# Kernel optimization log

Measured on AMD Instinct MI355X. Metric: run time of the kernel, lower is better.

Reference implementation:

```python
import jax, jax.numpy as jnp
import numpy as np

HEADS = 5 - 1  # 4 attention heads (GPSConv heads=4)


def _bn(x, g, b, eps=1e-5):
    # BatchNorm1d, training-mode math (biased variance), matches torch normalization
    mu = x.mean(0)
    var = x.var(0)
    return g * (x - mu) * jax.lax.rsqrt(var + eps) + b


def _forward(x, t, freqs, t_fc1_W, t_fc1_b, t_fc2_W, t_fc2_b, node_W, node_b,
             tproj_W, tproj_b, tcat_W, tcat_b, pen_g, pen_b, pel_W, pel_b,
             cat_W, cat_b, conv_Wg, gru_Wih, gru_bih, gru_Whh, gru_bhh,
             attn_Wqkv, attn_bqkv, attn_Wo, attn_bo, bn_g, bn_b,
             mlp_W1, mlp_b1, mlp_W2, mlp_b2, out_W, out_b):
    B, C, Hh, Ww = x.shape
    HD = node_W.shape[1]          # hidden_dim = 64
    DH = HD // HEADS              # per-head dim = 16
    WL = pen_g.shape[0]           # walk_length = 20

    xf = x.reshape(B, -1)                              # [B, D]
    h = xf @ node_W + node_b                           # node_proj

    # TimeEmbedding: t @ freqs -> sin/cos -> MLP, then time_proj
    tp = t.reshape(B, 1) * freqs.reshape(1, -1)        # [B, nf]
    two_pi = jnp.asarray(2.0 * np.pi, x.dtype)
    te = jnp.concatenate([jnp.sin(two_pi * tp), jnp.cos(two_pi * tp)], axis=-1)
    te = jax.nn.silu(te @ t_fc1_W + t_fc1_b) @ t_fc2_W + t_fc2_b
    h_time = te @ tproj_W + tproj_b
    h = jnp.concatenate([h, h_time], axis=-1) @ tcat_W + tcat_b  # time_cat_proj

    # Fully-connected graph incl. self-loops: A = 1 everywhere, deg = B.
    # Random-walk PE: P = A/deg has all entries 1/B; P is idempotent (P@P = P),
    # hence diag(P^k) = diag(P) = 1/B for every k in 1..walk_length.
    A = jnp.ones((B, B), x.dtype)
    P = A / A.sum(1, keepdims=True)
    pe = jnp.broadcast_to(jnp.diagonal(P)[:, None], (B, WL))
    pe = _bn(pe, pen_g, pen_b)                         # pe_norm (batch stats)
    h = jnp.concatenate([h, pe @ pel_W + pel_b], axis=-1) @ cat_W + cat_b

    inv_sqrt = jnp.asarray(1.0 / np.sqrt(DH), x.dtype)
    for l in range(conv_Wg.shape[0]):                  # 5 GPSConv layers
        # --- GatedGraphConv (num_layers=1): message, add-aggregate, GRU ---
        m = A @ (h @ conv_Wg[l])                       # sum of messages from all src nodes
        gi = m @ gru_Wih[l] + gru_bih[l]               # [B, 3H]
        gh = h @ gru_Whh[l] + gru_bhh[l]
        ir, iz, inn = jnp.split(gi, 3, axis=-1)
        hr, hz, hn = jnp.split(gh, 3, axis=-1)
        r = jax.nn.sigmoid(ir + hr)
        z = jax.nn.sigmoid(iz + hz)
        n = jnp.tanh(inn + r * hn)
        hc = (1.0 - z) * n + z * h                     # GRUCell output
        h1 = _bn(hc + h, bn_g[l, 0], bn_b[l, 0])       # residual + norm1

        # --- global multihead self-attention over the single dense batch ---
        qkv = h @ attn_Wqkv[l] + attn_bqkv[l]
        q, k, v = jnp.split(qkv, 3, axis=-1)
        q = q.reshape(B, HEADS, DH).transpose(1, 0, 2)  # [h, B, d]
        k = k.reshape(B, HEADS, DH).transpose(1, 0, 2)
        v = v.reshape(B, HEADS, DH).transpose(1, 0, 2)
        att = jax.nn.softmax(jnp.einsum('hqd,hkd->hqk', q, k) * inv_sqrt, axis=-1)
        o = jnp.einsum('hqk,hkd->hqd', att, v).transpose(1, 0, 2).reshape(B, HD)
        o = o @ attn_Wo[l] + attn_bo[l]
        h2 = _bn(o + h, bn_g[l, 1], bn_b[l, 1])        # residual + norm2

        s = h1 + h2
        s = s + (jax.nn.relu(s @ mlp_W1[l] + mlp_b1[l]) @ mlp_W2[l] + mlp_b2[l])
        h = _bn(s, bn_g[l, 2], bn_b[l, 2])             # norm3

    return (h @ out_W + out_b).reshape(B, C, Hh, Ww)


def setup_inputs() -> dict:
    key = jax.random.key(0)
    B, C, H, W = 2048, 4, 32, 32
    D = C * H * W                 # 4096
    HD, PE, WL, L = 64, 16, 20, 5
    NF, TH, TC = 8, 64, 64
    ks = iter(jax.random.split(key, 40))

    def rn(shape, s=0.05):
        return jax.random.normal(next(ks), shape, jnp.float32) * s

    return {
        'x': jax.random.normal(next(ks), (B, C, H, W), jnp.float32),
        't': jax.random.uniform(next(ks), (B,), jnp.float32),
        'freqs': rn((NF,), 1.0),
        't_fc1_W': rn((2 * NF, TH)), 't_fc1_b': rn((TH,)),
        't_fc2_W': rn((TH, TC)), 't_fc2_b': rn((TC,)),
        'node_W': rn((D, HD), 0.02), 'node_b': rn((HD,)),
        'tproj_W': rn((TC, HD)), 'tproj_b': rn((HD,)),
        'tcat_W': rn((2 * HD, HD)), 'tcat_b': rn((HD,)),
        'pen_g': jnp.ones((WL,), jnp.float32), 'pen_b': jnp.zeros((WL,), jnp.float32),
        'pel_W': rn((WL, PE)), 'pel_b': rn((PE,)),
        'cat_W': rn((HD + PE, HD)), 'cat_b': rn((HD,)),
        'conv_Wg': rn((L, HD, HD)),
        'gru_Wih': rn((L, HD, 3 * HD)), 'gru_bih': rn((L, 3 * HD)),
        'gru_Whh': rn((L, HD, 3 * HD)), 'gru_bhh': rn((L, 3 * HD)),
        'attn_Wqkv': rn((L, HD, 3 * HD)), 'attn_bqkv': rn((L, 3 * HD)),
        'attn_Wo': rn((L, HD, HD)), 'attn_bo': rn((L, HD)),
        'bn_g': jnp.ones((L, 3, HD), jnp.float32), 'bn_b': jnp.zeros((L, 3, HD), jnp.float32),
        'mlp_W1': rn((L, HD, 2 * HD)), 'mlp_b1': rn((L, 2 * HD)),
        'mlp_W2': rn((L, 2 * HD, HD)), 'mlp_b2': rn((L, HD)),
        'out_W': rn((HD, D)), 'out_b': rn((D,)),
    }


def reference(x, t, freqs, t_fc1_W, t_fc1_b, t_fc2_W, t_fc2_b, node_W, node_b,
              tproj_W, tproj_b, tcat_W, tcat_b, pen_g, pen_b, pel_W, pel_b,
              cat_W, cat_b, conv_Wg, gru_Wih, gru_bih, gru_Whh, gru_bhh,
              attn_Wqkv, attn_bqkv, attn_Wo, attn_bo, bn_g, bn_b,
              mlp_W1, mlp_b1, mlp_W2, mlp_b2, out_W, out_b):
    return _forward(x, t, freqs, t_fc1_W, t_fc1_b, t_fc2_W, t_fc2_b, node_W, node_b,
                    tproj_W, tproj_b, tcat_W, tcat_b, pen_g, pen_b, pel_W, pel_b,
                    cat_W, cat_b, conv_Wg, gru_Wih, gru_bih, gru_Whh, gru_bhh,
                    attn_Wqkv, attn_bqkv, attn_Wo, attn_bo, bn_g, bn_b,
                    mlp_W1, mlp_b1, mlp_W2, mlp_b2, out_W, out_b)
```

## Files before the change

### kernel.cpp

```cpp
#include <hip/hip_runtime.h>

#define NB 2048
#define HDM 64
#define NLAY 5

typedef __bf16 bf16x8 __attribute__((ext_vector_type(8)));
typedef float v4f __attribute__((ext_vector_type(4)));

__device__ __forceinline__ float sigmoidf_(float x){ return 1.f/(1.f+__expf(-x)); }
__device__ __forceinline__ float tanhfast_(float x){
  x = fminf(fmaxf(x, -15.f), 15.f);
  float e = __expf(2.f*x);
  return (e-1.f)/(e+1.f);
}
__device__ __forceinline__ unsigned short f2b_rne(float f){
  unsigned u = __float_as_uint(f);
  unsigned r = u + 0x7FFFu + ((u>>16)&1u);
  return (unsigned short)(r>>16);
}
__device__ __forceinline__ unsigned pk2(float a, float b){
  unsigned ua = (__float_as_uint(a) + 0x8000u) >> 16;
  unsigned ub = (__float_as_uint(b) + 0x8000u) & 0xFFFF0000u;
  return ua | ub;
}

__global__ __launch_bounds__(256) void k_pre(
    const float* __restrict__ x, const float* __restrict__ tt,
    const float* __restrict__ freqs,
    const float* __restrict__ fc1W, const float* __restrict__ fc1b,
    const float* __restrict__ fc2W, const float* __restrict__ fc2b,
    const float* __restrict__ tprojW, const float* __restrict__ tprojb,
    const float* __restrict__ nodeW,
    float* __restrict__ h0p, float* __restrict__ htime,
    float* __restrict__ zero_region)
{
  __shared__ float xs[16*260];
  __shared__ float tb0[128];
  __shared__ float tb1[128];
  const int t = threadIdx.x, blk = blockIdx.x;
  const int r = t>>6, c = t&63;

  if (blk == 0){
    for (int i = t; i < 320 + 1920; i += 256) zero_region[i] = 0.f;
  }

  {
    const int row = blk*2 + (r&1);
    const float tv = tt[row];
    if (r < 2){
      float te[16];
      #pragma unroll
      for (int j=0;j<8;++j){
        float sv, cv;
        __sincosf(6.28318530717958647692f*tv*freqs[j], &sv, &cv);
        te[j]=sv; te[j+8]=cv;
      }
      float a = fc1b[c];
      #pragma unroll
      for (int j=0;j<16;++j) a += te[j]*fc1W[j*64+c];
      tb0[r*64+c] = a*sigmoidf_(a);
    }
    __syncthreads();
    if (r < 2){
      float b2 = fc2b[c];
      #pragma unroll 8
      for (int k=0;k<64;++k) b2 += tb0[r*64+k]*fc2W[k*64+c];
      tb1[r*64+c] = b2;
    }
    __syncthreads();
    if (r < 2){
      float hti = tprojb[c];
      #pragma unroll 8
      for (int k=0;k<64;++k) hti += tb1[r*64+k]*tprojW[k*64+c];
      htime[row*64+c] = hti;
    }
  }

  const int rg = blk>>3, kq = blk&7;
  const int rows0 = rg*16, k0 = kq*512;
  const int col4 = (t&15)*4;
  const int rq4  = ((t>>4)&3)*4;
  const int ksub = (t>>6)*64;

  float4 a0={0,0,0,0}, a1={0,0,0,0}, a2={0,0,0,0}, a3={0,0,0,0};

  for (int ch=0; ch<2; ++ch){
    __syncthreads();
    #pragma unroll
    for (int i=0;i<4;++i){
      int fi = t + 256*i;
      int xr = fi>>6, kk = (fi&63)<<2;
      *(float4*)&xs[xr*260+kk] = *(const float4*)&x[(size_t)(rows0+xr)*4096 + k0 + ch*256 + kk];
    }
    __syncthreads();
    const float* wp = &nodeW[(size_t)(k0 + ch*256 + ksub)*64 + col4];
    const float* xp = &xs[rq4*260 + ksub];
    #pragma unroll 8
    for (int kk=0; kk<64; ++kk){
      float4 w  = *(const float4*)&wp[kk*64];
      float x0 = xp[kk];
      float x1 = xp[260+kk];
      float x2 = xp[520+kk];
      float x3 = xp[780+kk];
      a0.x += x0*w.x; a0.y += x0*w.y; a0.z += x0*w.z; a0.w += x0*w.w;
      a1.x += x1*w.x; a1.y += x1*w.y; a1.z += x1*w.z; a1.w += x1*w.w;
      a2.x += x2*w.x; a2.y += x2*w.y; a2.z += x2*w.z; a2.w += x2*w.w;
      a3.x += x3*w.x; a3.y += x3*w.y; a3.z += x3*w.z; a3.w += x3*w.w;
    }
  }
  __syncthreads();
  {
    const int kqi = t>>6;
    *(float4*)&xs[(kqi*16 + rq4 + 0)*64 + col4] = a0;
    *(float4*)&xs[(kqi*16 + rq4 + 1)*64 + col4] = a1;
    *(float4*)&xs[(kqi*16 + rq4 + 2)*64 + col4] = a2;
    *(float4*)&xs[(kqi*16 + rq4 + 3)*64 + col4] = a3;
  }
  __syncthreads();
  {
    const int row = t>>4, c4 = (t&15)*4;
    float4 s = {0,0,0,0};
    #pragma unroll
    for (int q=0;q<4;++q){
      float4 v = *(const float4*)&xs[(q*16+row)*64 + c4];
      s.x+=v.x; s.y+=v.y; s.z+=v.z; s.w+=v.w;
    }
    *(float4*)&h0p[(size_t)kq*(NB*HDM) + (rows0+row)*64 + c4] = s;
  }
}

__global__ __launch_bounds__(256) void k_assemble(
    const float* __restrict__ h0p, const float* __restrict__ htime,
    const float* __restrict__ nodeb,
    const float* __restrict__ tcatW, const float* __restrict__ tcatb,
    const float* __restrict__ penb, const float* __restrict__ pelW,
    const float* __restrict__ pelb,
    const float* __restrict__ catW, const float* __restrict__ catb,
    float* __restrict__ hbuf)
{
  __shared__ float sa[256];
  __shared__ float sb[256];
  __shared__ float cvec[64];
  const int t = threadIdx.x, blk = blockIdx.x;
  const int r = t>>6, c = t&63;
  const int row = blk*4 + r;

  if (r==0){
    float pl[16];
    #pragma unroll
    for (int j=0;j<16;++j){
      float a = pelb[j];
      for (int w=0;w<20;++w) a += penb[w]*pelW[w*16+j];
      pl[j]=a;
    }
    float a = catb[c];
    #pragma unroll
    for (int j=0;j<16;++j) a += pl[j]*catW[(64+j)*64+c];
    cvec[c]=a;
  }
  float h0 = nodeb[c];
  #pragma unroll
  for (int q=0;q<8;++q) h0 += h0p[(size_t)q*(NB*HDM) + row*64 + c];
  sa[t] = h0;
  sb[t] = htime[row*64+c];
  __syncthreads();
  float a = tcatb[c];
  #pragma unroll 4
  for (int k=0;k<64;++k){
    a += sa[r*64+k]*tcatW[k*64+c];
    a += sb[r*64+k]*tcatW[(64+k)*64+c];
  }
  __syncthreads();
  sa[t] = a;
  __syncthreads();
  float hv = cvec[c];
  #pragma unroll 8
  for (int k=0;k<64;++k) hv += sa[r*64+k]*catW[k*64+c];
  hbuf[row*64+c] = hv;
}

__global__ __launch_bounds__(256) void k_A(
    const float* __restrict__ smlp,
    const float* __restrict__ bnaccPrev,
    const float* __restrict__ gPrev, const float* __restrict__ bPrev,
    float* __restrict__ hbuf, float* __restrict__ hsumL,
    const float* __restrict__ Whh, const float* __restrict__ bhh,
    const float* __restrict__ Wq,  const float* __restrict__ bq,
    float* __restrict__ gh,
    unsigned short* __restrict__ Qb, unsigned short* __restrict__ Kb,
    unsigned short* __restrict__ Vt, int first)
{
  __shared__ float sa[8*64];
  const int t = threadIdx.x, blk = blockIdx.x;
  const int row0 = blk*8;

  #pragma unroll
  for (int i=0;i<2;++i){
    int idx = t + 256*i;
    int rl = idx>>6, c = idx&63;
    int row = row0 + rl;
    float hv;
    if (first){
      hv = hbuf[row*64+c];
    } else {
      float mu = bnaccPrev[256+c]*(1.f/NB);
      float va = bnaccPrev[320+c]*(1.f/NB) - mu*mu;
      hv = gPrev[c]*(smlp[row*64+c]-mu)*rsqrtf(va+1e-5f)+bPrev[c];
      hbuf[row*64+c] = hv;
    }
    sa[idx] = hv;
  }
  __syncthreads();
  if (t<64){
    float s = 0.f;
    #pragma unroll
    for (int rl=0;rl<8;++rl) s += sa[rl*64+t];
    atomicAdd(&hsumL[t], s);
  }
  if (t < 192){
    const int cc = t;
    float ag[8], aq[8];
    float bh = bhh[cc], bq_ = bq[cc];
    #pragma unroll
    for (int rl=0;rl<8;++rl){ ag[rl]=bh; aq[rl]=bq_; }
    #pragma unroll 4
    for (int k=0;k<64;++k){
      float wh = Whh[k*192+cc];
      float wq = Wq [k*192+cc];
      #pragma unroll
      for (int rl=0;rl<8;++rl){
        float hk = sa[rl*64+k];
        ag[rl] += hk*wh;
        aq[rl] += hk*wq;
      }
    }
    #pragma unroll
    for (int rl=0;rl<8;++rl){
      int rw = row0 + rl;
      gh[(size_t)rw*192+cc] = ag[rl];
      float aqv = aq[rl];
      if (cc < 64){
        int hd = cc>>4, dh = cc&15;
        size_t base = ((size_t)(hd<<11) + rw)*32;
        Qb[base+dh] = f2b_rne(aqv*0.25f);
        Qb[base+16+dh] = 0;
      } else if (cc < 128){
        int c2 = cc-64, hd = c2>>4, dh = c2&15;
        size_t base = ((size_t)(hd<<11) + rw)*32;
        Kb[base+dh] = f2b_rne(aqv);
        Kb[base+16+dh] = 0;
      } else {
        int c2 = cc-128, hd = c2>>4, dh = c2&15;
        Vt[((size_t)(hd*16+dh))*2048 + rw] = f2b_rne(aqv);
      }
    }
  }
}

__global__ __launch_bounds__(256) void k_attn(
    const unsigned short* __restrict__ Qb, const unsigned short* __restrict__ Kb,
    const unsigned short* __restrict__ Vt,
    float* __restrict__ o_out)
{
  __shared__ unsigned short Pl[4*640];
  __shared__ float Os[4*272];
  __shared__ float ms[64], ls[64];
  const int t = threadIdx.x;
  const int w = t>>6, lane = t&63;
  const int q15 = lane & 15, quad = lane >> 4;
  const int b = blockIdx.x;
  const int qt = b & 127, head = b>>7;
  const int qrow = qt*16 + q15;
  const int key00 = w*512;
  unsigned short* Plw = &Pl[w*640];

  const bf16x8 qf = *(const bf16x8*)&Qb[(((size_t)(head<<11))+qrow)*32 + quad*8];
  const unsigned short* Kb_h = Kb + ((size_t)(head<<11))*32;
  const unsigned short* Vrow = Vt + ((size_t)(head*16+q15))*2048;

  v4f O = {0.f,0.f,0.f,0.f};
  float m = -1e30f, lsum = 0.f;

  bf16x8 kf0 = *(const bf16x8*)&Kb_h[(size_t)(key00 + q15)*32 + quad*8];
  bf16x8 kf1 = *(const bf16x8*)&Kb_h[(size_t)(key00 + 16 + q15)*32 + quad*8];
  bf16x8 vf  = *(const bf16x8*)&Vrow[key00 + quad*8];

  for (int c=0; c<16; ++c){
    bf16x8 nk0, nk1, nv;
    if (c < 15){
      int nk = key00 + (c+1)*32;
      nk0 = *(const bf16x8*)&Kb_h[(size_t)(nk + q15)*32 + quad*8];
      nk1 = *(const bf16x8*)&Kb_h[(size_t)(nk + 16 + q15)*32 + quad*8];
      nv  = *(const bf16x8*)&Vrow[nk + quad*8];
    }
    v4f z = {0.f,0.f,0.f,0.f};
    v4f s0 = __builtin_amdgcn_mfma_f32_16x16x32_bf16(kf0, qf, z, 0,0,0);
    v4f s1 = __builtin_amdgcn_mfma_f32_16x16x32_bf16(kf1, qf, z, 0,0,0);
    float cmax = fmaxf(fmaxf(fmaxf(s0[0],s0[1]),fmaxf(s0[2],s0[3])),
                       fmaxf(fmaxf(s1[0],s1[1]),fmaxf(s1[2],s1[3])));
    cmax = fmaxf(cmax, __shfl_xor(cmax,16,64));
    cmax = fmaxf(cmax, __shfl_xor(cmax,32,64));
    float mnew = fmaxf(m, cmax);
    float alpha = __expf(m - mnew);
    float p0=__expf(s0[0]-mnew), p1=__expf(s0[1]-mnew), p2=__expf(s0[2]-mnew), p3=__expf(s0[3]-mnew);
    float p4=__expf(s1[0]-mnew), p5=__expf(s1[1]-mnew), p6=__expf(s1[2]-mnew), p7=__expf(s1[3]-mnew);
    lsum = alpha*lsum + ((p0+p1)+(p2+p3)+((p4+p5)+(p6+p7)));
    m = mnew;
    O[0]*=alpha; O[1]*=alpha; O[2]*=alpha; O[3]*=alpha;
    *(uint2*)&Plw[q15*40 + quad*4]      = make_uint2(pk2(p0,p1), pk2(p2,p3));
    *(uint2*)&Plw[q15*40 + 16 + quad*4] = make_uint2(pk2(p4,p5), pk2(p6,p7));
    asm volatile("s_waitcnt lgkmcnt(0)" ::: "memory");
    bf16x8 pf = *(const bf16x8*)&Plw[q15*40 + quad*8];
    O = __builtin_amdgcn_mfma_f32_16x16x32_bf16(vf, pf, O, 0,0,0);
    kf0 = nk0; kf1 = nk1; vf = nv;
  }
  lsum += __shfl_xor(lsum,16,64);
  lsum += __shfl_xor(lsum,32,64);
  #pragma unroll
  for (int j=0;j<4;++j) Os[w*272 + q15*17 + quad*4 + j] = O[j];
  if (quad==0){ ms[w*16+q15]=m; ls[w*16+q15]=lsum; }
  __syncthreads();
  {
    const int dh = t&15, q = t>>4;
    float m0=ms[q], m1=ms[16+q], m2=ms[32+q], m3=ms[48+q];
    float mm = fmaxf(fmaxf(m0,m1),fmaxf(m2,m3));
    float a0=__expf(m0-mm), a1=__expf(m1-mm), a2=__expf(m2-mm), a3=__expf(m3-mm);
    float ll = a0*ls[q]+a1*ls[16+q]+a2*ls[32+q]+a3*ls[48+q];
    float oo = a0*Os[q*17+dh] + a1*Os[272+q*17+dh] + a2*Os[544+q*17+dh] + a3*Os[816+q*17+dh];
    o_out[(size_t)(qt*16+q)*64 + head*16 + dh] = oo / ll;
  }
}

__global__ __launch_bounds__(256) void k_B2(
    const float* __restrict__ hbuf, const float* __restrict__ gh,
    const float* __restrict__ hsumL, const float* __restrict__ o_out,
    const float* __restrict__ Wg,   const float* __restrict__ Wih,
    const float* __restrict__ bih,  const float* __restrict__ Wo,
    const float* __restrict__ bo,
    float* __restrict__ s1, float* __restrict__ s2, float* __restrict__ bnaccL)
{
  __shared__ float sa[8*64];
  __shared__ float os[8*64];
  __shared__ float smv_[64];
  __shared__ float sgi[192];
  __shared__ float Sb1[8*64];
  __shared__ float Sb2[8*64];
  const int t = threadIdx.x, blk = blockIdx.x;
  const int row0 = blk*8;

  if (t<64){
    float a=0.f;
    #pragma unroll 8
    for (int k=0;k<64;++k) a += hsumL[k]*Wg[k*64+t];
    smv_[t]=a;
  }
  #pragma unroll
  for (int i=0;i<2;++i){
    int idx = t + 256*i;
    int rl = idx>>6, c = idx&63;
    sa[idx] = hbuf[(size_t)(row0+rl)*64+c];
    os[idx] = o_out[(size_t)(row0+rl)*64+c];
  }
  __syncthreads();
  if (t<192){
    float a = bih[t];
    #pragma unroll 8
    for (int k=0;k<64;++k) a += smv_[k]*Wih[k*192+t];
    sgi[t]=a;
  }
  __syncthreads();

  const int c = t&63, rg = t>>6;
  float o2a = bo[c], o2b = bo[c];
  #pragma unroll 4
  for (int k=0;k<64;++k){
    float w = Wo[k*64+c];
    o2a += os[(rg*2  )*64+k]*w;
    o2b += os[(rg*2+1)*64+k]*w;
  }
  #pragma unroll
  for (int i=0;i<2;++i){
    int rl = rg*2 + i;
    int row = row0 + rl;
    float o2 = i ? o2b : o2a;
    float hv = sa[rl*64+c];
    float s2v = o2 + hv;
    float ir = sgi[c]      + gh[(size_t)row*192+c];
    float iz = sgi[64+c]   + gh[(size_t)row*192+64+c];
    float inn = sgi[128+c];
    float hn  = gh[(size_t)row*192+128+c];
    float rr_ = sigmoidf_(ir);
    float zz  = sigmoidf_(iz);
    float nn  = tanhfast_(inn + rr_*hn);
    float s1v = (1.f-zz)*nn + zz*hv + hv;
    s1[(size_t)row*64+c] = s1v;
    s2[(size_t)row*64+c] = s2v;
    Sb1[rl*64+c] = s1v;
    Sb2[rl*64+c] = s2v;
  }
  __syncthreads();
  if (t<64){
    float a=0.f,aq=0.f,b=0.f,bq2=0.f;
    #pragma unroll
    for (int rl=0;rl<8;++rl){
      float v1 = Sb1[rl*64+t], v2 = Sb2[rl*64+t];
      a+=v1; aq+=v1*v1; b+=v2; bq2+=v2*v2;
    }
    atomicAdd(&bnaccL[t],a);     atomicAdd(&bnaccL[64+t],aq);
    atomicAdd(&bnaccL[128+t],b); atomicAdd(&bnaccL[192+t],bq2);
  }
}

__global__ __launch_bounds__(256) void k_C(
    const float* __restrict__ s1, const float* __restrict__ s2,
    const float* __restrict__ bngL, const float* __restrict__ bnbL,
    const float* __restrict__ W1, const float* __restrict__ b1,
    const float* __restrict__ W2, const float* __restrict__ b2,
    float* __restrict__ smlp, float* __restrict__ bnaccL)
{
  __shared__ float sa[8*64];
  __shared__ float sh[8*128];
  __shared__ float S2[8*64];
  const int t = threadIdx.x, blk = blockIdx.x;
  const int row0 = blk*8;

  #pragma unroll
  for (int i=0;i<2;++i){
    int idx = t + 256*i;
    int rl = idx>>6, c = idx&63;
    int row = row0 + rl;
    float mu1 = bnaccL[c]*(1.f/NB);
    float va1 = bnaccL[64+c]*(1.f/NB) - mu1*mu1;
    float mu2 = bnaccL[128+c]*(1.f/NB);
    float va2 = bnaccL[192+c]*(1.f/NB) - mu2*mu2;
    float h1 = bngL[c]*(s1[(size_t)row*64+c]-mu1)*rsqrtf(va1+1e-5f)+bnbL[c];
    float h2 = bngL[64+c]*(s2[(size_t)row*64+c]-mu2)*rsqrtf(va2+1e-5f)+bnbL[64+c];
    sa[idx] = h1+h2;
  }
  __syncthreads();
  {
    const int hj = t&127, rgq = t>>7;
    float a0v=b1[hj], a1v=b1[hj], a2v=b1[hj], a3v=b1[hj];
    #pragma unroll 4
    for (int k=0;k<64;++k){
      float w = W1[k*128+hj];
      a0v += sa[(rgq*4  )*64+k]*w;
      a1v += sa[(rgq*4+1)*64+k]*w;
      a2v += sa[(rgq*4+2)*64+k]*w;
      a3v += sa[(rgq*4+3)*64+k]*w;
    }
    sh[(rgq*4  )*128+hj] = fmaxf(a0v,0.f);
    sh[(rgq*4+1)*128+hj] = fmaxf(a1v,0.f);
    sh[(rgq*4+2)*128+hj] = fmaxf(a2v,0.f);
    sh[(rgq*4+3)*128+hj] = fmaxf(a3v,0.f);
  }
  __syncthreads();
  {
    const int c = t&63, rg = t>>6;
    float moa = b2[c], mob = b2[c];
    #pragma unroll 4
    for (int k=0;k<128;++k){
      float w = W2[k*64+c];
      moa += sh[(rg*2  )*128+k]*w;
      mob += sh[(rg*2+1)*128+k]*w;
    }
    #pragma unroll
    for (int i=0;i<2;++i){
      int rl = rg*2+i;
      float smv2 = sa[rl*64+c] + (i ? mob : moa);
      smlp[(size_t)(row0+rl)*64+c] = smv2;
      S2[rl*64+c] = smv2;
    }
  }
  __syncthreads();
  if (t<64){
    float a=0.f,aq=0.f;
    #pragma unroll
    for (int rl=0;rl<8;++rl){ float v=S2[rl*64+t]; a+=v; aq+=v*v; }
    atomicAdd(&bnaccL[256+t],a); atomicAdd(&bnaccL[320+t],aq);
  }
}

__global__ __launch_bounds__(256) void k_out(
  const float* __restrict__ smlp, const float* __restrict__ bnacc4,
  const float* __restrict__ g4, const float* __restrict__ b4,
  const float* __restrict__ outW, const float* __restrict__ outb,
  float* __restrict__ out)
{
  __shared__ float hsT[64*20];
  const int t = threadIdx.x, blk = blockIdx.x;
  const int rg = blk>>2, cg = blk&3;
  const int rows0 = rg*16;
  #pragma unroll
  for (int i=0;i<4;++i){
    int idx = t + 256*i;
    int k = idx&63, rr = idx>>6;
    float mu = bnacc4[256+k]*(1.f/NB);
    float va = bnacc4[320+k]*(1.f/NB)-mu*mu;
    hsT[k*20+rr] = g4[k]*(smlp[(size_t)(rows0+rr)*64+k]-mu)*rsqrtf(va+1e-5f)+b4[k];
  }
  __syncthreads();
  const int cc = cg*1024 + t*4;
  float4 acc[16];
  {
    float4 bv = *(const float4*)&outb[cc];
    #pragma unroll
    for (int rr=0;rr<16;++rr) acc[rr]=bv;
  }
  #pragma unroll 4
  for (int k=0;k<64;++k){
    float4 w = *(const float4*)&outW[(size_t)k*4096+cc];
    const float4* hp = (const float4*)&hsT[k*20];
    float4 h0=hp[0], h1=hp[1], h2=hp[2], h3=hp[3];
    acc[0].x+=h0.x*w.x;  acc[0].y+=h0.x*w.y;  acc[0].z+=h0.x*w.z;  acc[0].w+=h0.x*w.w;
    acc[1].x+=h0.y*w.x;  acc[1].y+=h0.y*w.y;  acc[1].z+=h0.y*w.z;  acc[1].w+=h0.y*w.w;
    acc[2].x+=h0.z*w.x;  acc[2].y+=h0.z*w.y;  acc[2].z+=h0.z*w.z;  acc[2].w+=h0.z*w.w;
    acc[3].x+=h0.w*w.x;  acc[3].y+=h0.w*w.y;  acc[3].z+=h0.w*w.z;  acc[3].w+=h0.w*w.w;
    acc[4].x+=h1.x*w.x;  acc[4].y+=h1.x*w.y;  acc[4].z+=h1.x*w.z;  acc[4].w+=h1.x*w.w;
    acc[5].x+=h1.y*w.x;  acc[5].y+=h1.y*w.y;  acc[5].z+=h1.y*w.z;  acc[5].w+=h1.y*w.w;
    acc[6].x+=h1.z*w.x;  acc[6].y+=h1.z*w.y;  acc[6].z+=h1.z*w.z;  acc[6].w+=h1.z*w.w;
    acc[7].x+=h1.w*w.x;  acc[7].y+=h1.w*w.y;  acc[7].z+=h1.w*w.z;  acc[7].w+=h1.w*w.w;
    acc[8].x+=h2.x*w.x;  acc[8].y+=h2.x*w.y;  acc[8].z+=h2.x*w.z;  acc[8].w+=h2.x*w.w;
    acc[9].x+=h2.y*w.x;  acc[9].y+=h2.y*w.y;  acc[9].z+=h2.y*w.z;  acc[9].w+=h2.y*w.w;
    acc[10].x+=h2.z*w.x; acc[10].y+=h2.z*w.y; acc[10].z+=h2.z*w.z; acc[10].w+=h2.z*w.w;
    acc[11].x+=h2.w*w.x; acc[11].y+=h2.w*w.y; acc[11].z+=h2.w*w.z; acc[11].w+=h2.w*w.w;
    acc[12].x+=h3.x*w.x; acc[12].y+=h3.x*w.y; acc[12].z+=h3.x*w.z; acc[12].w+=h3.x*w.w;
    acc[13].x+=h3.y*w.x; acc[13].y+=h3.y*w.y; acc[13].z+=h3.y*w.z; acc[13].w+=h3.y*w.w;
    acc[14].x+=h3.z*w.x; acc[14].y+=h3.z*w.y; acc[14].z+=h3.z*w.z; acc[14].w+=h3.z*w.w;
    acc[15].x+=h3.w*w.x; acc[15].y+=h3.w*w.y; acc[15].z+=h3.w*w.z; acc[15].w+=h3.w*w.w;
  }
  #pragma unroll
  for (int rr=0;rr<16;++rr)
    *(float4*)&out[(size_t)(rows0+rr)*4096+cc] = acc[rr];
}

extern "C" void kernel_launch(void* const* d_in, const int* in_sizes, int n_in,
                              void* d_out, int out_size, void* d_ws, size_t ws_size,
                              hipStream_t stream)
{
  (void)in_sizes; (void)n_in; (void)out_size; (void)ws_size;
  const float* x      = (const float*)d_in[0];
  const float* tt     = (const float*)d_in[1];
  const float* freqs  = (const float*)d_in[2];
  const float* fc1W   = (const float*)d_in[3];
  const float* fc1b   = (const float*)d_in[4];
  const float* fc2W   = (const float*)d_in[5];
  const float* fc2b   = (const float*)d_in[6];
  const float* nodeW  = (const float*)d_in[7];
  const float* nodeb  = (const float*)d_in[8];
  const float* tprojW = (const float*)d_in[9];
  const float* tprojb = (const float*)d_in[10];
  const float* tcatW  = (const float*)d_in[11];
  const float* tcatb  = (const float*)d_in[12];
  const float* penb   = (const float*)d_in[14];
  const float* pelW   = (const float*)d_in[15];
  const float* pelb   = (const float*)d_in[16];
  const float* catW   = (const float*)d_in[17];
  const float* catb   = (const float*)d_in[18];
  const float* convWg = (const float*)d_in[19];
  const float* gruWih = (const float*)d_in[20];
  const float* grubih = (const float*)d_in[21];
  const float* gruWhh = (const float*)d_in[22];
  const float* grubhh = (const float*)d_in[23];
  const float* Wqkv   = (const float*)d_in[24];
  const float* bqkv   = (const float*)d_in[25];
  const float* Wo     = (const float*)d_in[26];
  const float* bo     = (const float*)d_in[27];
  const float* bng    = (const float*)d_in[28];
  const float* bnb    = (const float*)d_in[29];
  const float* W1     = (const float*)d_in[30];
  const float* b1     = (const float*)d_in[31];
  const float* W2     = (const float*)d_in[32];
  const float* b2     = (const float*)d_in[33];
  const float* outW   = (const float*)d_in[34];
  const float* outb   = (const float*)d_in[35];

  float* ws = (float*)d_ws;
  float* htime = ws;
  float* hbuf  = htime + 131072;
  float* gh    = hbuf + 131072;
  float* s1    = gh + 393216;
  float* s2    = s1 + 131072;
  float* smlp  = s2 + 131072;
  float* o_out = smlp + 131072;
  float* hsum  = o_out + 131072;
  float* bnacc = hsum + 320;
  unsigned short* Qb = (unsigned short*)(bnacc + 1920);
  unsigned short* Kb = Qb + 262144;
  unsigned short* Vt = Kb + 262144;
  float* h0p  = (float*)(Vt + 65536);

  dim3 Blk(256);

  k_pre<<<dim3(1024), Blk, 0, stream>>>(x, tt, freqs, fc1W, fc1b, fc2W, fc2b,
                                        tprojW, tprojb, nodeW, h0p, htime, hsum);

  k_assemble<<<dim3(512), Blk, 0, stream>>>(h0p, htime, nodeb, tcatW, tcatb,
                                            penb, pelW, pelb, catW, catb, hbuf);

  for (int l=0; l<NLAY; ++l){
    const float* bnaccPrev = (l==0) ? bnacc : bnacc + (l-1)*384;
    const float* gPrev = (l==0) ? bng : bng + (l-1)*192 + 128;
    const float* bPrev = (l==0) ? bnb : bnb + (l-1)*192 + 128;
    k_A<<<dim3(256), Blk, 0, stream>>>(smlp, bnaccPrev, gPrev, bPrev,
                                       hbuf, hsum + l*64,
                                       gruWhh + l*12288, grubhh + l*192,
                                       Wqkv + l*12288, bqkv + l*192,
                                       gh, Qb, Kb, Vt, (l==0) ? 1 : 0);
    k_attn<<<dim3(512), Blk, 0, stream>>>(Qb, Kb, Vt, o_out);
    k_B2<<<dim3(256), Blk, 0, stream>>>(hbuf, gh, hsum + l*64, o_out,
                                        convWg + l*4096, gruWih + l*12288, grubih + l*192,
                                        Wo + l*4096, bo + l*64,
                                        s1, s2, bnacc + l*384);
    k_C<<<dim3(256), Blk, 0, stream>>>(s1, s2, bng + l*192, bnb + l*192,
                                       W1 + l*8192, b1 + l*128, W2 + l*8192, b2 + l*64,
                                       smlp, bnacc + l*384);
  }

  k_out<<<dim3(512), Blk, 0, stream>>>(smlp, bnacc + 4*384, bng + 896, bnb + 896,
                                       outW, outb, (float*)d_out);
}
```

Baseline: 523.5 us.

## Fuse attention into GRU/output kernel and fold assemble into first layer kernel

Removes k_assemble by computing the initial hidden state inside k_A on the first layer. Merges k_attn into k_B2 to form a 512-thread k_B, where each block handles 8 query rows across 4 heads with 2 key-split waves per head. The attention output no longer round-trips through global memory, and two launches per layer are removed. For layers after the first, the column sum of h is replaced by 2048*beta, since batch-normalised rows sum to N*beta. The cost is fewer blocks doing attention with half-empty MFMA tiles (8 of 16 query rows), which lowers attention parallelism.

```diff
diff --git a/kernel.cpp b/kernel.cpp
--- a/kernel.cpp
+++ b/kernel.cpp
@@ -78,9 +78,7 @@
 
   const int rg = blk>>3, kq = blk&7;
   const int rows0 = rg*16, k0 = kq*512;
-  const int col4 = (t&15)*4;
-  const int rq4  = ((t>>4)&3)*4;
-  const int ksub = (t>>6)*64;
+  const int col4 = (t&15)*4, rq4 = ((t>>4)&3)*4, ksub = (t>>6)*64;
 
   float4 a0={0,0,0,0}, a1={0,0,0,0}, a2={0,0,0,0}, a3={0,0,0,0};
 
@@ -98,10 +96,7 @@
     #pragma unroll 8
     for (int kk=0; kk<64; ++kk){
       float4 w  = *(const float4*)&wp[kk*64];
-      float x0 = xp[kk];
-      float x1 = xp[260+kk];
-      float x2 = xp[520+kk];
-      float x3 = xp[780+kk];
+      float x0 = xp[kk], x1 = xp[260+kk], x2 = xp[520+kk], x3 = xp[780+kk];
       a0.x += x0*w.x; a0.y += x0*w.y; a0.z += x0*w.z; a0.w += x0*w.w;
       a1.x += x1*w.x; a1.y += x1*w.y; a1.z += x1*w.z; a1.w += x1*w.w;
       a2.x += x2*w.x; a2.y += x2*w.y; a2.z += x2*w.z; a2.w += x2*w.w;
@@ -127,56 +122,6 @@
     }
     *(float4*)&h0p[(size_t)kq*(NB*HDM) + (rows0+row)*64 + c4] = s;
   }
-}
-
-__global__ __launch_bounds__(256) void k_assemble(
-    const float* __restrict__ h0p, const float* __restrict__ htime,
-    const float* __restrict__ nodeb,
-    const float* __restrict__ tcatW, const float* __restrict__ tcatb,
-    const float* __restrict__ penb, const float* __restrict__ pelW,
-    const float* __restrict__ pelb,
-    const float* __restrict__ catW, const float* __restrict__ catb,
-    float* __restrict__ hbuf)
-{
-  __shared__ float sa[256];
-  __shared__ float sb[256];
-  __shared__ float cvec[64];
-  const int t = threadIdx.x, blk = blockIdx.x;
-  const int r = t>>6, c = t&63;
-  const int row = blk*4 + r;
-
-  if (r==0){
-    float pl[16];
-    #pragma unroll
-    for (int j=0;j<16;++j){
-      float a = pelb[j];
-      for (int w=0;w<20;++w) a += penb[w]*pelW[w*16+j];
-      pl[j]=a;
-    }
-    float a = catb[c];
-    #pragma unroll
-    for (int j=0;j<16;++j) a += pl[j]*catW[(64+j)*64+c];
-    cvec[c]=a;
-  }
-  float h0 = nodeb[c];
-  #pragma unroll
-  for (int q=0;q<8;++q) h0 += h0p[(size_t)q*(NB*HDM) + row*64 + c];
-  sa[t] = h0;
-  sb[t] = htime[row*64+c];
-  __syncthreads();
-  float a = tcatb[c];
-  #pragma unroll 4
-  for (int k=0;k<64;++k){
-    a += sa[r*64+k]*tcatW[k*64+c];
-    a += sb[r*64+k]*tcatW[(64+k)*64+c];
-  }
-  __syncthreads();
-  sa[t] = a;
-  __syncthreads();
-  float hv = cvec[c];
-  #pragma unroll 8
-  for (int k=0;k<64;++k) hv += sa[r*64+k]*catW[k*64+c];
-  hbuf[row*64+c] = hv;
 }
 
 __global__ __launch_bounds__(256) void k_A(
@@ -188,35 +133,94 @@
     const float* __restrict__ Wq,  const float* __restrict__ bq,
     float* __restrict__ gh,
     unsigned short* __restrict__ Qb, unsigned short* __restrict__ Kb,
-    unsigned short* __restrict__ Vt, int first)
+    unsigned short* __restrict__ Vt,
+    const float* __restrict__ h0p, const float* __restrict__ htime,
+    const float* __restrict__ nodeb,
+    const float* __restrict__ tcatW, const float* __restrict__ tcatb,
+    const float* __restrict__ penb, const float* __restrict__ pelW,
+    const float* __restrict__ pelb,
+    const float* __restrict__ catW, const float* __restrict__ catb,
+    int first)
 {
   __shared__ float sa[8*64];
+  __shared__ float bufA[8*64];
+  __shared__ float bufB[8*64];
+  __shared__ float bufC[8*64];
+  __shared__ float cvec[64];
   const int t = threadIdx.x, blk = blockIdx.x;
   const int row0 = blk*8;
 
-  #pragma unroll
-  for (int i=0;i<2;++i){
-    int idx = t + 256*i;
-    int rl = idx>>6, c = idx&63;
-    int row = row0 + rl;
-    float hv;
-    if (first){
-      hv = hbuf[row*64+c];
-    } else {
+  if (first){
+    if (t < 64){
+      float pl[16];
+      #pragma unroll
+      for (int j=0;j<16;++j){
+        float a = pelb[j];
+        for (int w=0;w<20;++w) a += penb[w]*pelW[w*16+j];
+        pl[j]=a;
+      }
+      float a = catb[t];
+      #pragma unroll
+      for (int j=0;j<16;++j) a += pl[j]*catW[(64+j)*64+t];
+      cvec[t]=a;
+    }
+    #pragma unroll
+    for (int i=0;i<2;++i){
+      int idx = t + 256*i;
+      int rl = idx>>6, c = idx&63;
+      int row = row0 + rl;
+      float h0 = nodeb[c];
+      #pragma unroll
+      for (int q=0;q<8;++q) h0 += h0p[(size_t)q*(NB*HDM) + (size_t)row*64 + c];
+      bufA[idx] = h0;
+      bufB[idx] = htime[(size_t)row*64+c];
+    }
+    __syncthreads();
+    #pragma unroll
+    for (int i=0;i<2;++i){
+      int idx = t + 256*i;
+      int rl = idx>>6, c = idx&63;
+      float a = tcatb[c];
+      #pragma unroll 4
+      for (int k=0;k<64;++k){
+        a += bufA[rl*64+k]*tcatW[k*64+c];
+        a += bufB[rl*64+k]*tcatW[(64+k)*64+c];
+      }
+      bufC[idx] = a;
+    }
+    __syncthreads();
+    #pragma unroll
+    for (int i=0;i<2;++i){
+      int idx = t + 256*i;
+      int rl = idx>>6, c = idx&63;
+      float hv = cvec[c];
+      #pragma unroll 8
+      for (int k=0;k<64;++k) hv += bufC[rl*64+k]*catW[k*64+c];
+      sa[idx] = hv;
+      hbuf[(size_t)(row0+rl)*64+c] = hv;
+    }
+    __syncthreads();
+    if (t < 64){
+      float s = 0.f;
+      #pragma unroll
+      for (int rl=0;rl<8;++rl) s += sa[rl*64+t];
+      atomicAdd(&hsumL[t], s);
+    }
+  } else {
+    #pragma unroll
+    for (int i=0;i<2;++i){
+      int idx = t + 256*i;
+      int rl = idx>>6, c = idx&63;
+      int row = row0 + rl;
       float mu = bnaccPrev[256+c]*(1.f/NB);
       float va = bnaccPrev[320+c]*(1.f/NB) - mu*mu;
-      hv = gPrev[c]*(smlp[row*64+c]-mu)*rsqrtf(va+1e-5f)+bPrev[c];
-      hbuf[row*64+c] = hv;
-    }
-    sa[idx] = hv;
-  }
-  __syncthreads();
-  if (t<64){
-    float s = 0.f;
-    #pragma unroll
-    for (int rl=0;rl<8;++rl) s += sa[rl*64+t];
-    atomicAdd(&hsumL[t], s);
-  }
+      float hv = gPrev[c]*(smlp[(size_t)row*64+c]-mu)*rsqrtf(va+1e-5f)+bPrev[c];
+      hbuf[(size_t)row*64+c] = hv;
+      sa[idx] = hv;
+    }
+    __syncthreads();
+  }
+
   if (t < 192){
     const int cc = t;
     float ag[8], aq[8];
@@ -257,137 +261,129 @@
   }
 }
 
-__global__ __launch_bounds__(256) void k_attn(
+__global__ __launch_bounds__(512) void k_B(
+    const float* __restrict__ hbuf, const float* __restrict__ gh,
+    const float* __restrict__ hsumL, const float* __restrict__ bP3,
     const unsigned short* __restrict__ Qb, const unsigned short* __restrict__ Kb,
     const unsigned short* __restrict__ Vt,
-    float* __restrict__ o_out)
-{
-  __shared__ unsigned short Pl[4*640];
-  __shared__ float Os[4*272];
-  __shared__ float ms[64], ls[64];
-  const int t = threadIdx.x;
-  const int w = t>>6, lane = t&63;
-  const int q15 = lane & 15, quad = lane >> 4;
-  const int b = blockIdx.x;
-  const int qt = b & 127, head = b>>7;
-  const int qrow = qt*16 + q15;
-  const int key00 = w*512;
-  unsigned short* Plw = &Pl[w*640];
-
-  const bf16x8 qf = *(const bf16x8*)&Qb[(((size_t)(head<<11))+qrow)*32 + quad*8];
-  const unsigned short* Kb_h = Kb + ((size_t)(head<<11))*32;
-  const unsigned short* Vrow = Vt + ((size_t)(head*16+q15))*2048;
-
-  v4f O = {0.f,0.f,0.f,0.f};
-  float m = -1e30f, lsum = 0.f;
-
-  bf16x8 kf0 = *(const bf16x8*)&Kb_h[(size_t)(key00 + q15)*32 + quad*8];
-  bf16x8 kf1 = *(const bf16x8*)&Kb_h[(size_t)(key00 + 16 + q15)*32 + quad*8];
-  bf16x8 vf  = *(const bf16x8*)&Vrow[key00 + quad*8];
-
-  for (int c=0; c<16; ++c){
-    bf16x8 nk0, nk1, nv;
-    if (c < 15){
-      int nk = key00 + (c+1)*32;
-      nk0 = *(const bf16x8*)&Kb_h[(size_t)(nk + q15)*32 + quad*8];
-      nk1 = *(const bf16x8*)&Kb_h[(size_t)(nk + 16 + q15)*32 + quad*8];
-      nv  = *(const bf16x8*)&Vrow[nk + quad*8];
-    }
-    v4f z = {0.f,0.f,0.f,0.f};
-    v4f s0 = __builtin_amdgcn_mfma_f32_16x16x32_bf16(kf0, qf, z, 0,0,0);
-    v4f s1 = __builtin_amdgcn_mfma_f32_16x16x32_bf16(kf1, qf, z, 0,0,0);
-    float cmax = fmaxf(fmaxf(fmaxf(s0[0],s0[1]),fmaxf(s0[2],s0[3])),
-                       fmaxf(fmaxf(s1[0],s1[1]),fmaxf(s1[2],s1[3])));
-    cmax = fmaxf(cmax, __shfl_xor(cmax,16,64));
-    cmax = fmaxf(cmax, __shfl_xor(cmax,32,64));
-    float mnew = fmaxf(m, cmax);
-    float alpha = __expf(m - mnew);
-    float p0=__expf(s0[0]-mnew), p1=__expf(s0[1]-mnew), p2=__expf(s0[2]-mnew), p3=__expf(s0[3]-mnew);
-    float p4=__expf(s1[0]-mnew), p5=__expf(s1[1]-mnew), p6=__expf(s1[2]-mnew), p7=__expf(s1[3]-mnew);
-    lsum = alpha*lsum + ((p0+p1)+(p2+p3)+((p4+p5)+(p6+p7)));
-    m = mnew;
-    O[0]*=alpha; O[1]*=alpha; O[2]*=alpha; O[3]*=alpha;
-    *(uint2*)&Plw[q15*40 + quad*4]      = make_uint2(pk2(p0,p1), pk2(p2,p3));
-    *(uint2*)&Plw[q15*40 + 16 + quad*4] = make_uint2(pk2(p4,p5), pk2(p6,p7));
-    asm volatile("s_waitcnt lgkmcnt(0)" ::: "memory");
-    bf16x8 pf = *(const bf16x8*)&Plw[q15*40 + quad*8];
-    O = __builtin_amdgcn_mfma_f32_16x16x32_bf16(vf, pf, O, 0,0,0);
-    kf0 = nk0; kf1 = nk1; vf = nv;
-  }
-  lsum += __shfl_xor(lsum,16,64);
-  lsum += __shfl_xor(lsum,32,64);
-  #pragma unroll
-  for (int j=0;j<4;++j) Os[w*272 + q15*17 + quad*4 + j] = O[j];
-  if (quad==0){ ms[w*16+q15]=m; ls[w*16+q15]=lsum; }
-  __syncthreads();
-  {
-    const int dh = t&15, q = t>>4;
-    float m0=ms[q], m1=ms[16+q], m2=ms[32+q], m3=ms[48+q];
-    float mm = fmaxf(fmaxf(m0,m1),fmaxf(m2,m3));
-    float a0=__expf(m0-mm), a1=__expf(m1-mm), a2=__expf(m2-mm), a3=__expf(m3-mm);
-    float ll = a0*ls[q]+a1*ls[16+q]+a2*ls[32+q]+a3*ls[48+q];
-    float oo = a0*Os[q*17+dh] + a1*Os[272+q*17+dh] + a2*Os[544+q*17+dh] + a3*Os[816+q*17+dh];
-    o_out[(size_t)(qt*16+q)*64 + head*16 + dh] = oo / ll;
-  }
-}
-
-__global__ __launch_bounds__(256) void k_B2(
-    const float* __restrict__ hbuf, const float* __restrict__ gh,
-    const float* __restrict__ hsumL, const float* __restrict__ o_out,
     const float* __restrict__ Wg,   const float* __restrict__ Wih,
     const float* __restrict__ bih,  const float* __restrict__ Wo,
     const float* __restrict__ bo,
-    float* __restrict__ s1, float* __restrict__ s2, float* __restrict__ bnaccL)
+    float* __restrict__ s1, float* __restrict__ s2, float* __restrict__ bnaccL,
+    int first)
 {
-  __shared__ float sa[8*64];
-  __shared__ float os[8*64];
-  __shared__ float smv_[64];
-  __shared__ float sgi[192];
-  __shared__ float Sb1[8*64];
-  __shared__ float Sb2[8*64];
+  __shared__ float smv[64];
+  __shared__ float gi[192];
+  __shared__ unsigned short Pl[8*640];
+  __shared__ float Os[8*272];
+  __shared__ float ms[128], ls[128];
+  __shared__ float oL[512];
+  __shared__ float Sb1[512], Sb2[512];
   const int t = threadIdx.x, blk = blockIdx.x;
   const int row0 = blk*8;
 
-  if (t<64){
-    float a=0.f;
-    #pragma unroll 8
-    for (int k=0;k<64;++k) a += hsumL[k]*Wg[k*64+t];
-    smv_[t]=a;
-  }
-  #pragma unroll
-  for (int i=0;i<2;++i){
-    int idx = t + 256*i;
-    int rl = idx>>6, c = idx&63;
-    sa[idx] = hbuf[(size_t)(row0+rl)*64+c];
-    os[idx] = o_out[(size_t)(row0+rl)*64+c];
-  }
-  __syncthreads();
-  if (t<192){
+  if (t < 64){
+    float a = 0.f;
+    if (first){
+      #pragma unroll 8
+      for (int k=0;k<64;++k) a += hsumL[k]*Wg[k*64+t];
+    } else {
+      #pragma unroll 8
+      for (int k=0;k<64;++k) a += (2048.f*bP3[k])*Wg[k*64+t];
+    }
+    smv[t]=a;
+  }
+  __syncthreads();
+  if (t < 192){
     float a = bih[t];
     #pragma unroll 8
-    for (int k=0;k<64;++k) a += smv_[k]*Wih[k*192+t];
-    sgi[t]=a;
-  }
-  __syncthreads();
-
-  const int c = t&63, rg = t>>6;
-  float o2a = bo[c], o2b = bo[c];
-  #pragma unroll 4
-  for (int k=0;k<64;++k){
-    float w = Wo[k*64+c];
-    o2a += os[(rg*2  )*64+k]*w;
-    o2b += os[(rg*2+1)*64+k]*w;
-  }
-  #pragma unroll
-  for (int i=0;i<2;++i){
-    int rl = rg*2 + i;
-    int row = row0 + rl;
-    float o2 = i ? o2b : o2a;
-    float hv = sa[rl*64+c];
+    for (int k=0;k<64;++k) a += smv[k]*Wih[k*192+t];
+    gi[t]=a;
+  }
+
+  {
+    const int w = t>>6, lane = t&63;
+    const int q15 = lane&15, quad = lane>>4;
+    const int head = w>>1, e = w&1;
+    const int key00 = e*1024;
+    unsigned short* Plw = &Pl[w*640];
+
+    bf16x8 qf;
+    if (q15 < 8){
+      qf = *(const bf16x8*)&Qb[(((size_t)(head<<11)) + (row0+q15))*32 + quad*8];
+    } else {
+      #pragma unroll
+      for (int j=0;j<8;++j) qf[j] = (__bf16)0.0f;
+    }
+    const unsigned short* Kb_h = Kb + ((size_t)(head<<11))*32;
+    const unsigned short* Vrow = Vt + ((size_t)(head*16+q15))*2048;
+
+    v4f O = {0.f,0.f,0.f,0.f};
+    float m = -1e30f, lsum = 0.f;
+
+    bf16x8 kf0 = *(const bf16x8*)&Kb_h[(size_t)(key00 + q15)*32 + quad*8];
+    bf16x8 kf1 = *(const bf16x8*)&Kb_h[(size_t)(key00 + 16 + q15)*32 + quad*8];
+    bf16x8 vf  = *(const bf16x8*)&Vrow[key00 + quad*8];
+
+    for (int c=0; c<32; ++c){
+      bf16x8 nk0, nk1, nv;
+      if (c < 31){
+        int nk = key00 + (c+1)*32;
+        nk0 = *(const bf16x8*)&Kb_h[(size_t)(nk + q15)*32 + quad*8];
+        nk1 = *(const bf16x8*)&Kb_h[(size_t)(nk + 16 + q15)*32 + quad*8];
+        nv  = *(const bf16x8*)&Vrow[nk + quad*8];
+      }
+      v4f z = {0.f,0.f,0.f,0.f};
+      v4f sc0 = __builtin_amdgcn_mfma_f32_16x16x32_bf16(kf0, qf, z, 0,0,0);
+      v4f sc1 = __builtin_amdgcn_mfma_f32_16x16x32_bf16(kf1, qf, z, 0,0,0);
+      float cmax = fmaxf(fmaxf(fmaxf(sc0[0],sc0[1]),fmaxf(sc0[2],sc0[3])),
+                         fmaxf(fmaxf(sc1[0],sc1[1]),fmaxf(sc1[2],sc1[3])));
+      cmax = fmaxf(cmax, __shfl_xor(cmax,16,64));
+      cmax = fmaxf(cmax, __shfl_xor(cmax,32,64));
+      float mnew = fmaxf(m, cmax);
+      float alpha = __expf(m - mnew);
+      float p0=__expf(sc0[0]-mnew), p1=__expf(sc0[1]-mnew), p2=__expf(sc0[2]-mnew), p3=__expf(sc0[3]-mnew);
+      float p4=__expf(sc1[0]-mnew), p5=__expf(sc1[1]-mnew), p6=__expf(sc1[2]-mnew), p7=__expf(sc1[3]-mnew);
+      lsum = alpha*lsum + ((p0+p1)+(p2+p3)+((p4+p5)+(p6+p7)));
+      m = mnew;
+      O[0]*=alpha; O[1]*=alpha; O[2]*=alpha; O[3]*=alpha;
+      *(uint2*)&Plw[q15*40 + quad*4]      = make_uint2(pk2(p0,p1), pk2(p2,p3));
+      *(uint2*)&Plw[q15*40 + 16 + quad*4] = make_uint2(pk2(p4,p5), pk2(p6,p7));
+      asm volatile("s_waitcnt lgkmcnt(0)" ::: "memory");
+      bf16x8 pf = *(const bf16x8*)&Plw[q15*40 + quad*8];
+      O = __builtin_amdgcn_mfma_f32_16x16x32_bf16(vf, pf, O, 0,0,0);
+      kf0 = nk0; kf1 = nk1; vf = nv;
+    }
+    lsum += __shfl_xor(lsum,16,64);
+    lsum += __shfl_xor(lsum,32,64);
+    #pragma unroll
+    for (int j=0;j<4;++j) Os[w*272 + q15*17 + quad*4 + j] = O[j];
+    if (quad==0){ ms[w*16+q15]=m; ls[w*16+q15]=lsum; }
+  }
+  __syncthreads();
+  {
+    const int q = t>>6, c = t&63;
+    const int head = c>>4, dh = c&15;
+    const int w0 = head*2, w1 = w0+1;
+    float m0 = ms[w0*16+q], m1 = ms[w1*16+q];
+    float mm = fmaxf(m0,m1);
+    float a0 = __expf(m0-mm), a1 = __expf(m1-mm);
+    float ll = a0*ls[w0*16+q] + a1*ls[w1*16+q];
+    float oo = a0*Os[w0*272+q*17+dh] + a1*Os[w1*272+q*17+dh];
+    oL[q*64+c] = oo / ll;
+  }
+  __syncthreads();
+  {
+    const int c = t&63, rg = t>>6;
+    const int row = row0 + rg;
+    float o2 = bo[c];
+    #pragma unroll 8
+    for (int k=0;k<64;++k) o2 += oL[rg*64+k]*Wo[k*64+c];
+    float hv = hbuf[(size_t)row*64+c];
     float s2v = o2 + hv;
-    float ir = sgi[c]      + gh[(size_t)row*192+c];
-    float iz = sgi[64+c]   + gh[(size_t)row*192+64+c];
-    float inn = sgi[128+c];
+    float ir  = gi[c]      + gh[(size_t)row*192+c];
+    float iz  = gi[64+c]   + gh[(size_t)row*192+64+c];
+    float inn = gi[128+c];
     float hn  = gh[(size_t)row*192+128+c];
     float rr_ = sigmoidf_(ir);
     float zz  = sigmoidf_(iz);
@@ -395,11 +391,11 @@
     float s1v = (1.f-zz)*nn + zz*hv + hv;
     s1[(size_t)row*64+c] = s1v;
     s2[(size_t)row*64+c] = s2v;
-    Sb1[rl*64+c] = s1v;
-    Sb2[rl*64+c] = s2v;
-  }
-  __syncthreads();
-  if (t<64){
+    Sb1[rg*64+c] = s1v;
+    Sb2[rg*64+c] = s2v;
+  }
+  __syncthreads();
+  if (t < 64){
     float a=0.f,aq=0.f,b=0.f,bq2=0.f;
     #pragma unroll
     for (int rl=0;rl<8;++rl){
@@ -582,8 +578,7 @@
   float* s1    = gh + 393216;
   float* s2    = s1 + 131072;
   float* smlp  = s2 + 131072;
-  float* o_out = smlp + 131072;
-  float* hsum  = o_out + 131072;
+  float* hsum  = smlp + 131072;
   float* bnacc = hsum + 320;
   unsigned short* Qb = (unsigned short*)(bnacc + 1920);
   unsigned short* Kb = Qb + 262144;
@@ -595,23 +590,23 @@
   k_pre<<<dim3(1024), Blk, 0, stream>>>(x, tt, freqs, fc1W, fc1b, fc2W, fc2b,
                                         tprojW, tprojb, nodeW, h0p, htime, hsum);
 
-  k_assemble<<<dim3(512), Blk, 0, stream>>>(h0p, htime, nodeb, tcatW, tcatb,
-                                            penb, pelW, pelb, catW, catb, hbuf);
-
   for (int l=0; l<NLAY; ++l){
     const float* bnaccPrev = (l==0) ? bnacc : bnacc + (l-1)*384;
     const float* gPrev = (l==0) ? bng : bng + (l-1)*192 + 128;
     const float* bPrev = (l==0) ? bnb : bnb + (l-1)*192 + 128;
     k_A<<<dim3(256), Blk, 0, stream>>>(smlp, bnaccPrev, gPrev, bPrev,
-                                       hbuf, hsum + l*64,
+                                       hbuf, hsum,
                                        gruWhh + l*12288, grubhh + l*192,
                                        Wqkv + l*12288, bqkv + l*192,
-                                       gh, Qb, Kb, Vt, (l==0) ? 1 : 0);
-    k_attn<<<dim3(512), Blk, 0, stream>>>(Qb, Kb, Vt, o_out);
-    k_B2<<<dim3(256), Blk, 0, stream>>>(hbuf, gh, hsum + l*64, o_out,
-                                        convWg + l*4096, gruWih + l*12288, grubih + l*192,
-                                        Wo + l*4096, bo + l*64,
-                                        s1, s2, bnacc + l*384);
+                                       gh, Qb, Kb, Vt,
+                                       h0p, htime, nodeb, tcatW, tcatb,
+                                       penb, pelW, pelb, catW, catb,
+                                       (l==0) ? 1 : 0);
+    k_B<<<dim3(256), dim3(512), 0, stream>>>(hbuf, gh, hsum, bPrev,
+                                       Qb, Kb, Vt,
+                                       convWg + l*4096, gruWih + l*12288, grubih + l*192,
+                                       Wo + l*4096, bo + l*64,
+                                       s1, s2, bnacc + l*384, (l==0) ? 1 : 0);
     k_C<<<dim3(256), Blk, 0, stream>>>(s1, s2, bng + l*192, bnb + l*192,
                                        W1 + l*8192, b1 + l*128, W2 + l*8192, b2 + l*64,
                                        smlp, bnacc + l*384);
```

After: 534.1 us. 2.0% more time.
